# Optimization experiments

Measured on AMD Instinct MI355X. Metric: run time of the kernel, lower is better.

Reference implementation:

```python
import jax, jax.numpy as jnp
import numpy as np

ALPHA = 2.0
B, C, H, W = 4, 2, 256, 256
_INF = 1e9  # larger than any squared pixel distance (max ~ (H+W)^2)


def _dt1d(f):
    # exact 1D squared distance transform via brute-force min-convolution
    # d[i] = min_j f[j] + (i-j)^2, vectorized along the last axis
    n = f.shape[-1]
    i = jnp.arange(n, dtype=f.dtype)
    d2 = (i[:, None] - i[None, :]) ** 2  # [n_out, n_in]
    return jnp.min(f[..., None, :] + d2, axis=-1)


def _edt(mask):
    # scipy.ndimage.distance_transform_edt semantics:
    # distance from each nonzero (True) element to the nearest zero (False) element
    f = jnp.where(mask, jnp.float32(_INF), jnp.float32(0.0))
    f = _dt1d(f)  # pass along W
    f = jnp.swapaxes(_dt1d(jnp.swapaxes(f, -1, -2)), -1, -2)  # pass along H
    return jnp.sqrt(f)


def _distance_field(img):
    # img: (B, 1, H, W) float; field = edt(fg) + edt(bg), zeroed when no fg (matches fg_mask.any() guard)
    fg = img > 0.5
    field = _edt(fg) + _edt(~fg)
    has_fg = jnp.any(fg, axis=(1, 2, 3), keepdims=True)
    return jnp.where(has_fg, field, jnp.float32(0.0))


def setup_inputs() -> dict:
    key = jax.random.key(0)
    k1, k2 = jax.random.split(key)
    model_output = jax.random.normal(k1, (B, C, H, W), dtype=jnp.float32)
    ground_truth = (jax.random.uniform(k2, (B, 1, H, W)) > 0.5).astype(jnp.float32)
    return {"model_output": model_output, "ground_truth": ground_truth}


def reference(model_output, ground_truth):
    # argmax over channel dim -> binary label map (b, 1, H, W)
    pred = jnp.argmax(model_output, axis=1)[:, None, :, :].astype(jnp.float32)
    pred_dt = _distance_field(pred)
    gt_dt = _distance_field(ground_truth)
    # original detaches the error term (no_grad loss)
    err = jax.lax.stop_gradient((pred - ground_truth) ** 2)
    dist = pred_dt ** ALPHA + gt_dt ** ALPHA
    return jnp.mean(err * dist)
```

## Files before the change

kernel.cpp:

```cpp
#include <hip/hip_runtime.h>

#define NSIDE 256
#define HW    65536
#define NB    4
#define NMAP  8

typedef unsigned long long u64;

static const size_t ZZ_OFF    = 0;
static const size_t ROWFG_OFF = (size_t)NMAP * NSIDE * 4 * 8;
static const size_t PART_OFF  = ROWFG_OFF + (size_t)NMAP * NSIDE;

__global__ void k_bits(const float* __restrict__ mo, const float* __restrict__ gt,
                       u64* __restrict__ zz, unsigned char* __restrict__ rowFg) {
    int m = blockIdx.x >> 8;
    int y = blockIdx.x & 255;
    int x = threadIdx.x;
    int bit;
    if (m < NB) {
        float c0 = mo[(size_t)(m * 2 + 0) * HW + y * NSIDE + x];
        float c1 = mo[(size_t)(m * 2 + 1) * HW + y * NSIDE + x];
        bit = (c1 > c0) ? 1 : 0;
    } else {
        bit = (gt[(size_t)(m - NB) * HW + y * NSIDE + x] > 0.5f) ? 1 : 0;
    }
    u64 fg = __ballot(bit);
    __shared__ u64 s[4];
    int wid = x >> 6;
    if ((x & 63) == 0) {
        zz[((size_t)m * NSIDE + y) * 4 + wid] = fg;
        s[wid] = fg;
    }
    __syncthreads();
    if (x == 0)
        rowFg[m * NSIDE + y] = ((s[0] | s[1] | s[2] | s[3]) != 0ull) ? 1 : 0;
}

__device__ __forceinline__ int nbit(u64 z0, u64 z1, u64 z2, u64 z3,
                                    int xw, u64 loM, u64 hiM, int x) {
    u64 a0 = (xw == 0) ? (z0 & loM) : z0;
    u64 a1 = (xw < 1) ? 0ull : ((xw == 1) ? (z1 & loM) : z1);
    u64 a2 = (xw < 2) ? 0ull : ((xw == 2) ? (z2 & loM) : z2);
    u64 a3 = (xw < 3) ? 0ull : ((xw == 3) ? (z3 & loM) : z3);
    int msb = -(1 << 20);
    msb = a0 ? (63  - __builtin_clzll(a0)) : msb;
    msb = a1 ? (127 - __builtin_clzll(a1)) : msb;
    msb = a2 ? (191 - __builtin_clzll(a2)) : msb;
    msb = a3 ? (255 - __builtin_clzll(a3)) : msb;
    int dl = x - msb;
    u64 b0 = (xw > 0) ? 0ull : (z0 & hiM);
    u64 b1 = (xw > 1) ? 0ull : ((xw == 1) ? (z1 & hiM) : z1);
    u64 b2 = (xw > 2) ? 0ull : ((xw == 2) ? (z2 & hiM) : z2);
    u64 b3 = (xw == 3) ? (z3 & hiM) : z3;
    int lsb = 1 << 20;
    lsb = b3 ? (192 + __builtin_ctzll(b3)) : lsb;
    lsb = b2 ? (128 + __builtin_ctzll(b2)) : lsb;
    lsb = b1 ? (64  + __builtin_ctzll(b1)) : lsb;
    lsb = b0 ? (      __builtin_ctzll(b0)) : lsb;
    int dr = lsb - x;
    return dl < dr ? dl : dr;
}

__global__ void k_colreduce(const u64* __restrict__ zz, float* __restrict__ part) {
    int b = blockIdx.x >> 8;
    int x = blockIdx.x & 255;
    int y = threadIdx.x;
    const u64* zp = &zz[((size_t)b * NSIDE + y) * 4];
    const u64* zg = &zz[((size_t)(NB + b) * NSIDE + y) * 4];
    u64 p0 = zp[0], p1 = zp[1], p2 = zp[2], p3 = zp[3];
    u64 g0 = zg[0], g1 = zg[1], g2 = zg[2], g3 = zg[3];
    int xw = x >> 6, xb = x & 63;
    u64 loM = (2ull << xb) - 1ull;
    u64 hiM = ~0ull << xb;
    int dPf = nbit(~p0, ~p1, ~p2, ~p3, xw, loM, hiM, x);
    int dPb = nbit( p0,  p1,  p2,  p3, xw, loM, hiM, x);
    int dGf = nbit(~g0, ~g1, ~g2, ~g3, xw, loM, hiM, x);
    int dGb = nbit( g0,  g1,  g2,  g3, xw, loM, hiM, x);
    __shared__ float cPf[NSIDE], cPb[NSIDE], cGf[NSIDE], cGb[NSIDE];
    cPf[y] = (dPf > 255) ? 1e9f : (float)(dPf * dPf);
    cPb[y] = (dPb > 255) ? 1e9f : (float)(dPb * dPb);
    cGf[y] = (dGf > 255) ? 1e9f : (float)(dGf * dGf);
    cGb[y] = (dGb > 255) ? 1e9f : (float)(dGb * dGb);
    __syncthreads();
    u64 pw = (xw == 0) ? p0 : (xw == 1) ? p1 : (xw == 2) ? p2 : p3;
    u64 gw = (xw == 0) ? g0 : (xw == 1) ? g1 : (xw == 2) ? g2 : g3;
    int predBit = (int)((pw >> xb) & 1ull);
    int gtBit   = (int)((gw >> xb) & 1ull);
    float e = (predBit != gtBit) ? 1.0f : 0.0f;
    float bPf = cPf[y], bPb = cPb[y], bGf = cGf[y], bGb = cGb[y];
    if (e == 0.0f) { bPf = 0.0f; bPb = 0.0f; bGf = 0.0f; bGb = 0.0f; }
    float fr = 0.0f;
    for (int r = 1; r < NSIDE; ++r) {
        fr += 1.0f;
        float drr = fr * fr;
        float bmax = fmaxf(fmaxf(bPf, bPb), fmaxf(bGf, bGb));
        if (__all(drr >= bmax)) break;
        int jm = y - r, jp = y + r;
        int jmc = jm < 0 ? 0 : jm;
        int jpc = jp > (NSIDE - 1) ? (NSIDE - 1) : jp;
        float aPf = cPf[jmc], aPb = cPb[jmc], aGf = cGf[jmc], aGb = cGb[jmc];
        float qPf = cPf[jpc], qPb = cPb[jpc], qGf = cGf[jpc], qGb = cGb[jpc];
        if (jm < 0) { aPf = 3e9f; aPb = 3e9f; aGf = 3e9f; aGb = 3e9f; }
        if (jp > NSIDE - 1) { qPf = 3e9f; qPb = 3e9f; qGf = 3e9f; qGb = 3e9f; }
        bPf = fminf(bPf, fminf(aPf, qPf) + drr);
        bPb = fminf(bPb, fminf(aPb, qPb) + drr);
        bGf = fminf(bGf, fminf(aGf, qGf) + drr);
        bGb = fminf(bGb, fminf(aGb, qGb) + drr);
    }
    float sP = e * (bPf + bPb);
    float sG = e * (bGf + bGb);
#pragma unroll
    for (int off = 32; off > 0; off >>= 1) {
        sP += __shfl_down(sP, off, 64);
        sG += __shfl_down(sG, off, 64);
    }
    __shared__ float rP[4], rG[4];
    int wid = threadIdx.x >> 6;
    if ((threadIdx.x & 63) == 0) { rP[wid] = sP; rG[wid] = sG; }
    __syncthreads();
    if (threadIdx.x == 0) {
        part[b * NSIDE + x]        = rP[0] + rP[1] + rP[2] + rP[3];
        part[(NB + b) * NSIDE + x] = rG[0] + rG[1] + rG[2] + rG[3];
    }
}

__global__ void k_final(const unsigned char* __restrict__ rowFg,
                        const float* __restrict__ part,
                        float* __restrict__ out) {
    int tid = threadIdx.x;
    int lane = tid & 63, w = tid >> 6;
    __shared__ int hasFg[NMAP];
    __shared__ float red[NMAP];
    if (tid < NMAP) hasFg[tid] = 0;
    __syncthreads();
    u64 v = ((const u64*)rowFg)[tid];
    if (v) atomicOr(&hasFg[tid >> 5], 1);
#pragma unroll
    for (int k = 0; k < 2; ++k) {
        int m = 2 * w + k;
        float4 f = ((const float4*)part)[m * 64 + lane];
        float s = f.x + f.y + f.z + f.w;
#pragma unroll
        for (int off = 32; off > 0; off >>= 1) s += __shfl_down(s, off, 64);
        if (lane == 0) red[m] = s;
    }
    __syncthreads();
    if (tid == 0) {
        double t = 0.0;
#pragma unroll
        for (int m = 0; m < NMAP; ++m)
            if (hasFg[m]) t += (double)red[m];
        out[0] = (float)(t * (1.0 / (double)(NB * HW)));
    }
}

extern "C" void kernel_launch(void* const* d_in, const int* in_sizes, int n_in,
                              void* d_out, int out_size, void* d_ws, size_t ws_size,
                              hipStream_t stream) {
    const float* mo = (const float*)d_in[0];
    const float* gt = (const float*)d_in[1];
    float* out = (float*)d_out;
    char* ws = (char*)d_ws;

    u64* zz              = (u64*)(ws + ZZ_OFF);
    unsigned char* rowFg = (unsigned char*)(ws + ROWFG_OFF);
    float* part          = (float*)(ws + PART_OFF);

    hipLaunchKernelGGL(k_bits,      dim3(NMAP * 256), dim3(256), 0, stream, mo, gt, zz, rowFg);
    hipLaunchKernelGGL(k_colreduce, dim3(NB * 256),   dim3(256), 0, stream, zz, part);
    hipLaunchKernelGGL(k_final,     dim3(1),          dim3(256), 0, stream, rowFg, part, out);
}
```

Measured before the change: 64.62 us.

## Fuse column reduction and final sum with last-block atomic, transpose bit layout

New measurement: 72.01 us. 11.4% more time.

```diff
diff --git a/kernel.cpp b/kernel.cpp
--- a/kernel.cpp
+++ b/kernel.cpp
@@ -4,15 +4,16 @@
 #define HW    65536
 #define NB    4
 #define NMAP  8
+#define NBLK2 128
 
 typedef unsigned long long u64;
 
-static const size_t ZZ_OFF    = 0;
-static const size_t ROWFG_OFF = (size_t)NMAP * NSIDE * 4 * 8;
-static const size_t PART_OFF  = ROWFG_OFF + (size_t)NMAP * NSIDE;
+static const size_t ZZ_OFF   = 0;
+static const size_t CNT_OFF  = (size_t)NMAP * 4 * NSIDE * 8;
+static const size_t SLOT_OFF = CNT_OFF + 64;
 
 __global__ void k_bits(const float* __restrict__ mo, const float* __restrict__ gt,
-                       u64* __restrict__ zz, unsigned char* __restrict__ rowFg) {
+                       u64* __restrict__ zzw, int* __restrict__ cnt) {
     int m = blockIdx.x >> 8;
     int y = blockIdx.x & 255;
     int x = threadIdx.x;
@@ -25,15 +26,9 @@
         bit = (gt[(size_t)(m - NB) * HW + y * NSIDE + x] > 0.5f) ? 1 : 0;
     }
     u64 fg = __ballot(bit);
-    __shared__ u64 s[4];
-    int wid = x >> 6;
-    if ((x & 63) == 0) {
-        zz[((size_t)m * NSIDE + y) * 4 + wid] = fg;
-        s[wid] = fg;
-    }
-    __syncthreads();
-    if (x == 0)
-        rowFg[m * NSIDE + y] = ((s[0] | s[1] | s[2] | s[3]) != 0ull) ? 1 : 0;
+    if ((x & 63) == 0)
+        zzw[((size_t)m * 4 + (x >> 6)) * NSIDE + y] = fg;
+    if (blockIdx.x == 0 && x == 0) *cnt = 0;
 }
 
 __device__ __forceinline__ int nbit(u64 z0, u64 z1, u64 z2, u64 z3,
@@ -61,96 +56,111 @@
     return dl < dr ? dl : dr;
 }
 
-__global__ void k_colreduce(const u64* __restrict__ zz, float* __restrict__ part) {
-    int b = blockIdx.x >> 8;
-    int x = blockIdx.x & 255;
-    int y = threadIdx.x;
-    const u64* zp = &zz[((size_t)b * NSIDE + y) * 4];
-    const u64* zg = &zz[((size_t)(NB + b) * NSIDE + y) * 4];
-    u64 p0 = zp[0], p1 = zp[1], p2 = zp[2], p3 = zp[3];
-    u64 g0 = zg[0], g1 = zg[1], g2 = zg[2], g3 = zg[3];
-    int xw = x >> 6, xb = x & 63;
-    u64 loM = (2ull << xb) - 1ull;
-    u64 hiM = ~0ull << xb;
-    int dPf = nbit(~p0, ~p1, ~p2, ~p3, xw, loM, hiM, x);
-    int dPb = nbit( p0,  p1,  p2,  p3, xw, loM, hiM, x);
-    int dGf = nbit(~g0, ~g1, ~g2, ~g3, xw, loM, hiM, x);
-    int dGb = nbit( g0,  g1,  g2,  g3, xw, loM, hiM, x);
-    __shared__ float cPf[NSIDE], cPb[NSIDE], cGf[NSIDE], cGb[NSIDE];
-    cPf[y] = (dPf > 255) ? 1e9f : (float)(dPf * dPf);
-    cPb[y] = (dPb > 255) ? 1e9f : (float)(dPb * dPb);
-    cGf[y] = (dGf > 255) ? 1e9f : (float)(dGf * dGf);
-    cGb[y] = (dGb > 255) ? 1e9f : (float)(dGb * dGb);
-    __syncthreads();
-    u64 pw = (xw == 0) ? p0 : (xw == 1) ? p1 : (xw == 2) ? p2 : p3;
-    u64 gw = (xw == 0) ? g0 : (xw == 1) ? g1 : (xw == 2) ? g2 : g3;
-    int predBit = (int)((pw >> xb) & 1ull);
-    int gtBit   = (int)((gw >> xb) & 1ull);
-    float e = (predBit != gtBit) ? 1.0f : 0.0f;
-    float bPf = cPf[y], bPb = cPb[y], bGf = cGf[y], bGb = cGb[y];
-    if (e == 0.0f) { bPf = 0.0f; bPb = 0.0f; bGf = 0.0f; bGb = 0.0f; }
-    float fr = 0.0f;
-    for (int r = 1; r < NSIDE; ++r) {
-        fr += 1.0f;
-        float drr = fr * fr;
-        float bmax = fmaxf(fmaxf(bPf, bPb), fmaxf(bGf, bGb));
-        if (__all(drr >= bmax)) break;
-        int jm = y - r, jp = y + r;
-        int jmc = jm < 0 ? 0 : jm;
-        int jpc = jp > (NSIDE - 1) ? (NSIDE - 1) : jp;
-        float aPf = cPf[jmc], aPb = cPb[jmc], aGf = cGf[jmc], aGb = cGb[jmc];
-        float qPf = cPf[jpc], qPb = cPb[jpc], qGf = cGf[jpc], qGb = cGb[jpc];
-        if (jm < 0) { aPf = 3e9f; aPb = 3e9f; aGf = 3e9f; aGb = 3e9f; }
-        if (jp > NSIDE - 1) { qPf = 3e9f; qPb = 3e9f; qGf = 3e9f; qGb = 3e9f; }
-        bPf = fminf(bPf, fminf(aPf, qPf) + drr);
-        bPb = fminf(bPb, fminf(aPb, qPb) + drr);
-        bGf = fminf(bGf, fminf(aGf, qGf) + drr);
-        bGb = fminf(bGb, fminf(aGb, qGb) + drr);
+__global__ __launch_bounds__(1024) void k_colfinal(const u64* __restrict__ zzw,
+                                                   float* __restrict__ slot,
+                                                   int* __restrict__ cnt,
+                                                   float* __restrict__ out) {
+    int b    = blockIdx.x >> 5;
+    int xch  = blockIdx.x & 31;
+    int g    = threadIdx.x >> 8;
+    int y    = threadIdx.x & 255;
+    int wv   = threadIdx.x >> 6;
+    int lane = threadIdx.x & 63;
+
+    u64 p0 = zzw[((size_t)(b * 4) + 0) * NSIDE + y];
+    u64 p1 = zzw[((size_t)(b * 4) + 1) * NSIDE + y];
+    u64 p2 = zzw[((size_t)(b * 4) + 2) * NSIDE + y];
+    u64 p3 = zzw[((size_t)(b * 4) + 3) * NSIDE + y];
+    u64 q0 = zzw[((size_t)((NB + b) * 4) + 0) * NSIDE + y];
+    u64 q1 = zzw[((size_t)((NB + b) * 4) + 1) * NSIDE + y];
+    u64 q2 = zzw[((size_t)((NB + b) * 4) + 2) * NSIDE + y];
+    u64 q3 = zzw[((size_t)((NB + b) * 4) + 3) * NSIDE + y];
+
+    __shared__ float cPf[4][NSIDE], cPb[4][NSIDE], cGf[4][NSIDE], cGb[4][NSIDE];
+    __shared__ float rP[16], rG[16];
+    __shared__ unsigned char oP[16], oG[16];
+    __shared__ int lastFlag;
+    __shared__ float fin[2];
+
+    int aP = __any(((p0 | p1 | p2 | p3) != 0ull) ? 1 : 0);
+    int aG = __any(((q0 | q1 | q2 | q3) != 0ull) ? 1 : 0);
+    if (lane == 0) { oP[wv] = aP ? 1 : 0; oG[wv] = aG ? 1 : 0; }
+
+    float accP = 0.0f, accG = 0.0f;
+    for (int round = 0; round < 2; ++round) {
+        int x  = xch * 8 + round * 4 + g;
+        int xw = x >> 6, xb = x & 63;
+        u64 loM = (2ull << xb) - 1ull;
+        u64 hiM = ~0ull << xb;
+        int dPf = nbit(~p0, ~p1, ~p2, ~p3, xw, loM, hiM, x);
+        int dPb = nbit( p0,  p1,  p2,  p3, xw, loM, hiM, x);
+        int dGf = nbit(~q0, ~q1, ~q2, ~q3, xw, loM, hiM, x);
+        int dGb = nbit( q0,  q1,  q2,  q3, xw, loM, hiM, x);
+        cPf[g][y] = (dPf > 255) ? 1e9f : (float)(dPf * dPf);
+        cPb[g][y] = (dPb > 255) ? 1e9f : (float)(dPb * dPb);
+        cGf[g][y] = (dGf > 255) ? 1e9f : (float)(dGf * dGf);
+        cGb[g][y] = (dGb > 255) ? 1e9f : (float)(dGb * dGb);
+        __syncthreads();
+        u64 pw = (xw == 0) ? p0 : (xw == 1) ? p1 : (xw == 2) ? p2 : p3;
+        u64 qw = (xw == 0) ? q0 : (xw == 1) ? q1 : (xw == 2) ? q2 : q3;
+        float e = (((pw >> xb) & 1ull) != ((qw >> xb) & 1ull)) ? 1.0f : 0.0f;
+        float bPf = cPf[g][y], bPb = cPb[g][y], bGf = cGf[g][y], bGb = cGb[g][y];
+        if (e == 0.0f) { bPf = 0.0f; bPb = 0.0f; bGf = 0.0f; bGb = 0.0f; }
+        float fr = 0.0f;
+        for (int r = 1; r < NSIDE; ++r) {
+            fr += 1.0f;
+            float drr = fr * fr;
+            float bmax = fmaxf(fmaxf(bPf, bPb), fmaxf(bGf, bGb));
+            if (__all(drr >= bmax)) break;
+            int jm = y - r, jp = y + r;
+            int jmc = jm < 0 ? 0 : jm;
+            int jpc = jp > (NSIDE - 1) ? (NSIDE - 1) : jp;
+            float aPf = cPf[g][jmc], aPb = cPb[g][jmc], aGf = cGf[g][jmc], aGb = cGb[g][jmc];
+            float ePf = cPf[g][jpc], ePb = cPb[g][jpc], eGf = cGf[g][jpc], eGb = cGb[g][jpc];
+            if (jm < 0)         { aPf = 3e9f; aPb = 3e9f; aGf = 3e9f; aGb = 3e9f; }
+            if (jp > NSIDE - 1) { ePf = 3e9f; ePb = 3e9f; eGf = 3e9f; eGb = 3e9f; }
+            bPf = fminf(bPf, fminf(aPf, ePf) + drr);
+            bPb = fminf(bPb, fminf(aPb, ePb) + drr);
+            bGf = fminf(bGf, fminf(aGf, eGf) + drr);
+            bGb = fminf(bGb, fminf(aGb, eGb) + drr);
+        }
+        float sP = e * (bPf + bPb);
+        float sG = e * (bGf + bGb);
+#pragma unroll
+        for (int off = 32; off > 0; off >>= 1) {
+            sP += __shfl_down(sP, off, 64);
+            sG += __shfl_down(sG, off, 64);
+        }
+        if (lane == 0) { rP[wv] = sP; rG[wv] = sG; }
+        __syncthreads();
+        if (threadIdx.x == 0) {
+#pragma unroll
+            for (int i = 0; i < 16; ++i) { accP += rP[i]; accG += rG[i]; }
+        }
+        __syncthreads();
     }
-    float sP = e * (bPf + bPb);
-    float sG = e * (bGf + bGb);
+
+    if (threadIdx.x == 0) {
+        int hP = 0, hG = 0;
 #pragma unroll
-    for (int off = 32; off > 0; off >>= 1) {
-        sP += __shfl_down(sP, off, 64);
-        sG += __shfl_down(sG, off, 64);
-    }
-    __shared__ float rP[4], rG[4];
-    int wid = threadIdx.x >> 6;
-    if ((threadIdx.x & 63) == 0) { rP[wid] = sP; rG[wid] = sG; }
-    __syncthreads();
-    if (threadIdx.x == 0) {
-        part[b * NSIDE + x]        = rP[0] + rP[1] + rP[2] + rP[3];
-        part[(NB + b) * NSIDE + x] = rG[0] + rG[1] + rG[2] + rG[3];
-    }
-}
-
-__global__ void k_final(const unsigned char* __restrict__ rowFg,
-                        const float* __restrict__ part,
-                        float* __restrict__ out) {
-    int tid = threadIdx.x;
-    int lane = tid & 63, w = tid >> 6;
-    __shared__ int hasFg[NMAP];
-    __shared__ float red[NMAP];
-    if (tid < NMAP) hasFg[tid] = 0;
-    __syncthreads();
-    u64 v = ((const u64*)rowFg)[tid];
-    if (v) atomicOr(&hasFg[tid >> 5], 1);
-#pragma unroll
-    for (int k = 0; k < 2; ++k) {
-        int m = 2 * w + k;
-        float4 f = ((const float4*)part)[m * 64 + lane];
-        float s = f.x + f.y + f.z + f.w;
-#pragma unroll
-        for (int off = 32; off > 0; off >>= 1) s += __shfl_down(s, off, 64);
-        if (lane == 0) red[m] = s;
+        for (int i = 0; i < 16; ++i) { hP |= oP[i]; hG |= oG[i]; }
+        slot[blockIdx.x] = (hP ? accP : 0.0f) + (hG ? accG : 0.0f);
+        __threadfence();
+        int old = atomicAdd(cnt, 1);
+        lastFlag = (old == NBLK2 - 1) ? 1 : 0;
     }
     __syncthreads();
-    if (tid == 0) {
-        double t = 0.0;
+    if (lastFlag) {
+        __threadfence();
+        if (threadIdx.x < NBLK2) {
+            float s = slot[threadIdx.x];
 #pragma unroll
-        for (int m = 0; m < NMAP; ++m)
-            if (hasFg[m]) t += (double)red[m];
-        out[0] = (float)(t * (1.0 / (double)(NB * HW)));
+            for (int off = 32; off > 0; off >>= 1) s += __shfl_down(s, off, 64);
+            if (lane == 0) fin[wv] = s;
+        }
+        __syncthreads();
+        if (threadIdx.x == 0)
+            out[0] = (fin[0] + fin[1]) * (1.0f / (float)(NB * HW));
     }
 }
 
@@ -162,11 +172,10 @@
     float* out = (float*)d_out;
     char* ws = (char*)d_ws;
 
-    u64* zz              = (u64*)(ws + ZZ_OFF);
-    unsigned char* rowFg = (unsigned char*)(ws + ROWFG_OFF);
-    float* part          = (float*)(ws + PART_OFF);
+    u64* zzw    = (u64*)(ws + ZZ_OFF);
+    int* cnt    = (int*)(ws + CNT_OFF);
+    float* slot = (float*)(ws + SLOT_OFF);
 
-    hipLaunchKernelGGL(k_bits,      dim3(NMAP * 256), dim3(256), 0, stream, mo, gt, zz, rowFg);
-    hipLaunchKernelGGL(k_colreduce, dim3(NB * 256),   dim3(256), 0, stream, zz, part);
-    hipLaunchKernelGGL(k_final,     dim3(1),          dim3(256), 0, stream, rowFg, part, out);
+    hipLaunchKernelGGL(k_bits,     dim3(NMAP * 256), dim3(256),  0, stream, mo, gt, zzw, cnt);
+    hipLaunchKernelGGL(k_colfinal, dim3(NBLK2),      dim3(1024), 0, stream, zzw, slot, cnt, out);
 }
```
